# Performance work log

Hardware: AMD Instinct MI355X
Metric: run time of the kernel (lower is better)

The kernel has to match this reference:

```python
import jax, jax.numpy as jnp
import numpy as np

BS, DIM, EMB_DIM, SRC, TDEC, NEMB = 64, 512, 512, 400, 100, 50257


def intra_attention(h_t, h, W_attn):
    # h_t: [bs, dim]; h: [n, bs, dim]; W_attn: [dim, dim]
    n, bs, dim = h.shape
    # Faithful to torch .view([bs, dim, n]) on a contiguous [n, bs, dim]
    # tensor: raw row-major memory reinterpretation (NOT a transpose).
    hv = jnp.reshape(h, (bs, dim, n))  # [bs, dim, n]
    # E_t = (h_t @ W) [bs,1,dim] bmm hv [bs,dim,n] -> [bs, n]
    E = jnp.einsum('bd,bdn->bn', h_t @ W_attn, hv)
    # sum-normalized (non-softmax) score, eq. (4)
    A = E / jnp.sum(E, axis=1, keepdims=True)  # [bs, n]
    C = jnp.einsum('bdn,bn->bd', hv, A)        # [bs, dim]
    return A, C


def pointer_generator(ae_t, ce_t, hd_t, cd_t, W_emb, W_proj, W_u, b_u, b_out):
    # c_cat: [3*dim, bs]
    c_cat = jnp.concatenate((hd_t, ce_t, cd_t), axis=1).T
    # p_switch: [bs]
    p_switch = jax.nn.sigmoid(W_u @ c_cat + b_u).squeeze(0)
    # shared-embedding output projection, sect 2.4
    W_out = jnp.tanh(W_emb @ W_proj)           # [n_emb, 3*dim]
    logits = W_out @ c_cat + b_out             # [n_emb, bs]
    p_vocab = jax.nn.softmax(logits, axis=0)   # softmax over vocab
    p_gen = ((1.0 - p_switch) * p_vocab).T     # [bs, n_emb]
    p_copy = p_switch[:, None] * ae_t          # [bs, src]
    return p_gen, p_copy


def setup_inputs() -> dict:
    key = jax.random.key(0)
    ks = jax.random.split(key, 12)
    inp = {
        'h_t': jax.random.uniform(ks[0], (BS, DIM), dtype=jnp.float32),
        'h_enc': jax.random.uniform(ks[1], (SRC, BS, DIM), dtype=jnp.float32),
        'h_dec': jax.random.uniform(ks[2], (TDEC, BS, DIM), dtype=jnp.float32),
        'x': jax.random.randint(ks[3], (SRC, BS, 1), 0, NEMB, dtype=jnp.int64) if jax.config.jax_enable_x64 else jax.random.randint(ks[3], (SRC, BS, 1), 0, NEMB, dtype=jnp.int32),
        # positive attention weights keep the sum-normalized score well-conditioned
        'W_attn_enc': jax.random.uniform(ks[4], (DIM, DIM), dtype=jnp.float32, maxval=0.05),
        'W_attn_dec': jax.random.uniform(ks[5], (DIM, DIM), dtype=jnp.float32, maxval=0.05),
        'W_emb': jax.random.normal(ks[6], (NEMB, EMB_DIM), dtype=jnp.float32) * 0.02,
        'W_proj': jax.random.normal(ks[7], (EMB_DIM, 3 * DIM), dtype=jnp.float32) * 0.02,
        'W_u': jax.random.normal(ks[8], (1, 3 * DIM), dtype=jnp.float32) * 0.02,
        'b_u': jnp.zeros((1,), dtype=jnp.float32),
        'b_out': jnp.zeros((NEMB, 1), dtype=jnp.float32),
    }
    return inp


def reference(h_t, h_enc, h_dec, x, W_attn_enc, W_attn_dec, W_emb, W_proj, W_u, b_u, b_out):
    # one decode step of ReinforcedDecoder: enc attn + dec attn + pointer-gen
    ae_t, ce_t = intra_attention(h_t, h_enc, W_attn_enc)
    ad_t, cd_t = intra_attention(h_t, h_dec, W_attn_dec)
    p_gen, p_copy = pointer_generator(ae_t, ce_t, h_t, cd_t,
                                      W_emb, W_proj, W_u, b_u, b_out)
    return p_gen, p_copy
```

## Files before the change

kernel.cpp:

```cpp
#include <hip/hip_runtime.h>
#include <math.h>

typedef __attribute__((ext_vector_type(8))) short bf16x8;
typedef __attribute__((ext_vector_type(4))) float f32x4;
typedef __attribute__((ext_vector_type(4))) float f4v;

#define BS   64
#define DIM  512
#define SRC  400
#define TDEC 100
#define NEMB 50257
#define K3   1536

#define WS_Q     0
#define WS_EENC  65536
#define WS_EDEC  91136
#define WS_CENC  97536
#define WS_CDEC  130304
#define WS_ESUM  163072
#define WS_PSW   163200
#define WS_SMAX  163264
#define WS_SSUM  163520
#define WS_WPT   163776
#define WS_CCF   556992
#define WS_ZBEG  WS_CENC
#define WS_ZCNT  (WS_WPT - WS_CENC)

__device__ __forceinline__ ushort f2bf(float x) {
    union { float f; unsigned u; } v; v.f = x;
    unsigned r = (v.u + 0x7FFFu + ((v.u >> 16) & 1u)) >> 16;
    return (ushort)r;
}
__device__ __forceinline__ bf16x8 pack8v(f4v a, f4v b) {
    union { ushort us[8]; bf16x8 v; } p;
    p.us[0] = f2bf(a.x); p.us[1] = f2bf(a.y); p.us[2] = f2bf(a.z); p.us[3] = f2bf(a.w);
    p.us[4] = f2bf(b.x); p.us[5] = f2bf(b.y); p.us[6] = f2bf(b.z); p.us[7] = f2bf(b.w);
    return p.v;
}
__device__ __forceinline__ float pade_tanh(float x) {
    const float x2 = x * x;
    const float num = x * fmaf(x2, 1.0f / 15.0f, 1.0f);
    const float den = fmaf(x2, 0.4f, 1.0f);
    return num * __frcp_rn(den);
}
__device__ __forceinline__ void gl2lds16(const void* g, void* l) {
    __builtin_amdgcn_global_load_lds(
        (const __attribute__((address_space(1))) unsigned int*)g,
        (__attribute__((address_space(3))) unsigned int*)l, 16, 0, 0);
}

__global__ __launch_bounds__(256) void k_prep(const float* __restrict__ h_t,
                                              const float* __restrict__ Wenc,
                                              const float* __restrict__ Wdec,
                                              const float* __restrict__ Wp,
                                              float* __restrict__ ws) {
    __shared__ float sh[128 * 68];
    const int tid = threadIdx.x;
    if (blockIdx.x < 32) {
        const int which = blockIdx.x >> 4;
        const int c0 = (blockIdx.x & 15) * 32;
        const float* W = which ? Wdec : Wenc;
        float* q = ws + WS_Q + which * (BS * DIM);
        float* hS = sh;
        float* WSm = sh + 64 * 65;
        const int c = tid & 31, bg = tid >> 5;
        float acc[8] = {0.f, 0.f, 0.f, 0.f, 0.f, 0.f, 0.f, 0.f};
        for (int kc = 0; kc < 8; ++kc) {
            __syncthreads();
            #pragma unroll
            for (int r = 0; r < 16; ++r) {
                const int idx = r * 256 + tid;
                const int b = idx >> 6, k = idx & 63;
                hS[b * 65 + k] = h_t[b * DIM + kc * 64 + k];
            }
            #pragma unroll
            for (int r = 0; r < 8; ++r) {
                const int idx = r * 256 + tid;
                const int k = idx >> 5, cc = idx & 31;
                WSm[k * 33 + cc] = W[(size_t)(kc * 64 + k) * DIM + c0 + cc];
            }
            __syncthreads();
            #pragma unroll 8
            for (int k = 0; k < 64; ++k) {
                const float wv = WSm[k * 33 + c];
                #pragma unroll
                for (int bb = 0; bb < 8; ++bb)
                    acc[bb] = fmaf(hS[(bg * 8 + bb) * 65 + k], wv, acc[bb]);
            }
        }
        #pragma unroll
        for (int bb = 0; bb < 8; ++bb)
            q[(bg * 8 + bb) * DIM + c0 + c] = acc[bb];
    } else {
        const int bid = blockIdx.x - 32;
        const int t = bid >> 2, c = bid & 3;
        float (*T32)[68] = (float (*)[68])sh;
        #pragma unroll
        for (int p = 0; p < 8; ++p) {
            const int idx = p * 256 + tid;
            const int kk = idx >> 4, s = idx & 15;
            const float4 v = *(const float4*)(Wp + (size_t)(c * 128 + kk) * K3 + t * 64 + s * 4);
            T32[kk][s * 4 + 0] = v.x; T32[kk][s * 4 + 1] = v.y;
            T32[kk][s * 4 + 2] = v.z; T32[kk][s * 4 + 3] = v.w;
        }
        __syncthreads();
        char* dst = (char*)(ws + WS_WPT) + (size_t)bid * 16384;
        #pragma unroll
        for (int p = 0; p < 4; ++p) {
            const int fid = p * 256 + tid;
            const int lane = fid & 63;
            const int J = (fid >> 6) & 3;
            const int ks = fid >> 8;
            const int j = J * 16 + (lane & 15);
            const int k0 = ks * 32 + (lane >> 4) * 8;
            f4v a, b;
            a.x = T32[k0 + 0][j]; a.y = T32[k0 + 1][j];
            a.z = T32[k0 + 2][j]; a.w = T32[k0 + 3][j];
            b.x = T32[k0 + 4][j]; b.y = T32[k0 + 5][j];
            b.z = T32[k0 + 6][j]; b.w = T32[k0 + 7][j];
            *(bf16x8*)(dst + fid * 16) = pack8v(a, b);
        }
    }
}

#define IC 16
__global__ __launch_bounds__(256) void k_attn(const float* __restrict__ h_enc,
                                              const float* __restrict__ h_dec,
                                              float* __restrict__ ws) {
    const int b = blockIdx.x, which = blockIdx.y, z = blockIdx.z;
    const int tid = threadIdx.x;
    const int n   = which ? TDEC : SRC;
    const int per = which ? (TDEC / 4) : (SRC / 4);
    const int i_begin = z * per, i_end = i_begin + per;
    const float* h  = which ? h_dec : h_enc;
    const float* q  = ws + WS_Q + which * (BS * DIM) + b * DIM;
    float* wsE      = ws + (which ? WS_EDEC : WS_EENC) + b * n;
    float* Cws      = ws + (which ? WS_CDEC : WS_CENC) + b * DIM;
    const float* hb = h + (size_t)b * DIM * n;

    __shared__ float hS[DIM * (IC + 1)];
    __shared__ float qs[DIM];
    __shared__ float Ered[256];
    __shared__ float Es[IC];

    qs[tid] = q[tid];
    qs[tid + 256] = q[tid + 256];

    const int ii = tid & (IC - 1);
    const int dg = tid >> 4;
    float c0 = 0.f, c1 = 0.f, esum = 0.f;

    for (int i0 = i_begin; i0 < i_end; i0 += IC) {
        const int ic = min(IC, i_end - i0);
        __syncthreads();
        #pragma unroll 8
        for (int idx = tid; idx < DIM * IC; idx += 256) {
            const int d = idx >> 4, i = idx & (IC - 1);
            hS[d * (IC + 1) + i] = (i < ic) ? hb[(size_t)d * n + i0 + i] : 0.f;
        }
        __syncthreads();
        float p = 0.f;
        #pragma unroll 8
        for (int d = dg * 32; d < dg * 32 + 32; ++d) p += qs[d] * hS[d * (IC + 1) + ii];
        Ered[dg * IC + ii] = p;
        __syncthreads();
        if (tid < IC) {
            float e = 0.f;
            #pragma unroll
            for (int g = 0; g < 16; ++g) e += Ered[g * IC + tid];
            Es[tid] = e;
            esum += e;
            if (tid < ic) wsE[i0 + tid] = e;
        }
        __syncthreads();
        #pragma unroll
        for (int i = 0; i < IC; ++i) {
            const float e = Es[i];
            c0 += hS[tid * (IC + 1) + i] * e;
            c1 += hS[(tid + 256) * (IC + 1) + i] * e;
        }
    }
    atomicAdd(&Cws[tid], c0);
    atomicAdd(&Cws[tid + 256], c1);
    __syncthreads();
    if (tid < IC) Ered[tid] = esum;
    __syncthreads();
    if (tid == 0) {
        float s = 0.f;
        #pragma unroll
        for (int g = 0; g < IC; ++g) s += Ered[g];
        atomicAdd(&ws[WS_ESUM + which * 64 + b], s);
    }
}

__global__ void k_pswitch(const float* __restrict__ h_t,
                          const float* __restrict__ W_u,
                          const float* __restrict__ b_u,
                          float* __restrict__ out_copy,
                          float* __restrict__ ws) {
    const int b = blockIdx.x, tid = threadIdx.x;
    const float invE = 1.f / ws[WS_ESUM + b];
    const float invD = 1.f / ws[WS_ESUM + 64 + b];
    const float* Ce = ws + WS_CENC + b * DIM;
    const float* Cd = ws + WS_CDEC + b * DIM;
    ushort* ccF = (ushort*)(ws + WS_CCF);
    __shared__ float red[256];
    const int nb = b >> 4, bl = b & 15;
    float part = 0.f;
    #pragma unroll
    for (int r = 0; r < 6; ++r) {
        const int j = tid + r * 256;
        float v = (j < DIM) ? h_t[b * DIM + j]
                            : ((j < 2 * DIM) ? Ce[j - DIM] * invE : Cd[j - 2 * DIM] * invD);
        const int t = j >> 6, jj = j & 63;
        const int kc = jj >> 5, lsub = (jj >> 3) & 3, e = jj & 7;
        ccF[t * 4096 + kc * 2048 + nb * 512 + (lsub * 16 + bl) * 8 + e] = f2bf(v);
        part += W_u[j] * v;
    }
    red[tid] = part;
    __syncthreads();
    for (int s = 128; s > 0; s >>= 1) {
        if (tid < s) red[tid] += red[tid + s];
        __syncthreads();
    }
    const float ps = 1.f / (1.f + expf(-(red[0] + b_u[0])));
    if (tid == 0) ws[WS_PSW + b] = ps;
    const float* Ee = ws + WS_EENC + b * SRC;
    for (int i = tid; i < SRC; i += 256) out_copy[b * SRC + i] = ps * Ee[i] * invE;
}

#define VB 128
#define WAITV(N) asm volatile("s_waitcnt vmcnt(" #N ")" ::: "memory")
__global__ __launch_bounds__(256, 2) void k_bigmm(const float* __restrict__ We,
                                                  const float* __restrict__ ws,
                                                  const float* __restrict__ b_out,
                                                  float* __restrict__ out) {
    __shared__ __align__(16) char smem[57344];
    const char* wptb = (const char*)(ws + WS_WPT);
    const char* ccfb = (const char*)(ws + WS_CCF);

    const int tid  = threadIdx.x;
    const int w    = tid >> 6, lane = tid & 63;
    const int lrow = lane & 15, lgrp = lane >> 4;
    const int vw   = blockIdx.x * VB + w * 32;
    const int row0 = vw + lrow, row1 = vw + 16 + lrow;
    char* ccL   = smem + 32768;
    char* tbase = smem + 40960 + w * 4096;
    const int swz = (lrow & 7) << 4;

    #pragma unroll
    for (int p = 0; p < 2; ++p) {
        const char* src = wptb + (size_t)p * 16384 + tid * 16;
        char* dst = smem + p * 16384 + tid * 16;
        #pragma unroll
        for (int rnd = 0; rnd < 4; ++rnd) gl2lds16(src + rnd * 4096, dst + rnd * 4096);
    }

    bf16x8 A0[16], A1[16];
    if (row0 < NEMB) {
        const f4v* p = (const f4v*)(We + (size_t)row0 * DIM + lgrp * 8);
        #pragma unroll
        for (int f = 0; f < 16; ++f)
            A0[f] = pack8v(__builtin_nontemporal_load(p + f * 8),
                           __builtin_nontemporal_load(p + f * 8 + 1));
    } else {
        #pragma unroll
        for (int f = 0; f < 16; ++f) A0[f] = (bf16x8){0, 0, 0, 0, 0, 0, 0, 0};
    }
    if (row1 < NEMB) {
        const f4v* p = (const f4v*)(We + (size_t)row1 * DIM + lgrp * 8);
        #pragma unroll
        for (int f = 0; f < 16; ++f)
            A1[f] = pack8v(__builtin_nontemporal_load(p + f * 8),
                           __builtin_nontemporal_load(p + f * 8 + 1));
    } else {
        #pragma unroll
        for (int f = 0; f < 16; ++f) A1[f] = (bf16x8){0, 0, 0, 0, 0, 0, 0, 0};
    }

    f32x4 La0[4], La1[4], Ta0[4], Ta1[4];
    #pragma unroll
    for (int i = 0; i < 4; ++i) {
        La0[i] = (f32x4){0.f, 0.f, 0.f, 0.f}; La1[i] = (f32x4){0.f, 0.f, 0.f, 0.f};
        Ta0[i] = (f32x4){0.f, 0.f, 0.f, 0.f}; Ta1[i] = (f32x4){0.f, 0.f, 0.f, 0.f};
    }

    for (int it = 0; it < 8; ++it) {
        #pragma unroll
        for (int u = 0; u < 12; ++u) {
            const int i = it * 12 + u;
            if (u == 11)           { if (it == 7) { WAITV(0); } else { WAITV(4); } }
            else if ((u & 3) == 1) { WAITV(6); }
            else                   { WAITV(4); }
            __builtin_amdgcn_s_barrier();
            {
                const char* bp = smem + (u & 1) * 16384 + lane * 16;
                __builtin_amdgcn_s_setprio(1);
                #pragma unroll
                for (int ks = 0; ks < 4; ++ks) {
                    const bf16x8 b0 = *(const bf16x8*)(bp + ks * 4096);
                    const bf16x8 b1 = *(const bf16x8*)(bp + ks * 4096 + 1024);
                    const bf16x8 b2 = *(const bf16x8*)(bp + ks * 4096 + 2048);
                    const bf16x8 b3 = *(const bf16x8*)(bp + ks * 4096 + 3072);
                    Ta0[0] = __builtin_amdgcn_mfma_f32_16x16x32_bf16(A0[(u & 3) * 4 + ks], b0, Ta0[0], 0, 0, 0);
                    Ta1[0] = __builtin_amdgcn_mfma_f32_16x16x32_bf16(A1[(u & 3) * 4 + ks], b0, Ta1[0], 0, 0, 0);
                    Ta0[1] = __builtin_amdgcn_mfma_f32_16x16x32_bf16(A0[(u & 3) * 4 + ks], b1, Ta0[1], 0, 0, 0);
                    Ta1[1] = __builtin_amdgcn_mfma_f32_16x16x32_bf16(A1[(u & 3) * 4 + ks], b1, Ta1[1], 0, 0, 0);
                    Ta0[2] = __builtin_amdgcn_mfma_f32_16x16x32_bf16(A0[(u & 3) * 4 + ks], b2, Ta0[2], 0, 0, 0);
                    Ta1[2] = __builtin_amdgcn_mfma_f32_16x16x32_bf16(A1[(u & 3) * 4 + ks], b2, Ta1[2], 0, 0, 0);
                    Ta0[3] = __builtin_amdgcn_mfma_f32_16x16x32_bf16(A0[(u & 3) * 4 + ks], b3, Ta0[3], 0, 0, 0);
                    Ta1[3] = __builtin_amdgcn_mfma_f32_16x16x32_bf16(A1[(u & 3) * 4 + ks], b3, Ta1[3], 0, 0, 0);
                }
                __builtin_amdgcn_s_setprio(0);
            }
            if ((u & 3) == 3) {
                #pragma unroll
                for (int nj = 0; nj < 4; ++nj) {
                    const int j = nj * 16 + lrow;
                    #pragma unroll
                    for (int r = 0; r < 4; ++r) {
                        const int v = lgrp * 4 + r;
                        *(ushort*)(tbase + v * 128 + ((j * 2) ^ ((v & 7) << 4))) =
                            f2bf(pade_tanh(Ta0[nj][r]));
                        *(ushort*)(tbase + (16 + v) * 128 + ((j * 2) ^ ((v & 7) << 4))) =
                            f2bf(pade_tanh(Ta1[nj][r]));
                    }
                }
                __builtin_amdgcn_s_setprio(1);
                #pragma unroll
                for (int kc = 0; kc < 2; ++kc) {
                    const bf16x8 tf0 = *(const bf16x8*)(tbase + lrow * 128 +
                                                        ((kc * 64 + lgrp * 16) ^ swz));
                    const bf16x8 tf1 = *(const bf16x8*)(tbase + (16 + lrow) * 128 +
                                                        ((kc * 64 + lgrp * 16) ^ swz));
                    const char* cb = ccL + kc * 4096 + lane * 16;
                    const bf16x8 c0 = *(const bf16x8*)(cb);
                    const bf16x8 c1 = *(const bf16x8*)(cb + 1024);
                    const bf16x8 c2 = *(const bf16x8*)(cb + 2048);
                    const bf16x8 c3 = *(const bf16x8*)(cb + 3072);
                    La0[0] = __builtin_amdgcn_mfma_f32_16x16x32_bf16(tf0, c0, La0[0], 0, 0, 0);
                    La1[0] = __builtin_amdgcn_mfma_f32_16x16x32_bf16(tf1, c0, La1[0], 0, 0, 0);
                    La0[1] = __builtin_amdgcn_mfma_f32_16x16x32_bf16(tf0, c1, La0[1], 0, 0, 0);
                    La1[1] = __builtin_amdgcn_mfma_f32_16x16x32_bf16(tf1, c1, La1[1], 0, 0, 0);
                    La0[2] = __builtin_amdgcn_mfma_f32_16x16x32_bf16(tf0, c2, La0[2], 0, 0, 0);
                    La1[2] = __builtin_amdgcn_mfma_f32_16x16x32_bf16(tf1, c2, La1[2], 0, 0, 0);
                    La0[3] = __builtin_amdgcn_mfma_f32_16x16x32_bf16(tf0, c3, La0[3], 0, 0, 0);
                    La1[3] = __builtin_amdgcn_mfma_f32_16x16x32_bf16(tf1, c3, La1[3], 0, 0, 0);
                }
                __builtin_amdgcn_s_setprio(0);
                #pragma unroll
                for (int z = 0; z < 4; ++z) {
                    Ta0[z] = (f32x4){0.f, 0.f, 0.f, 0.f};
                    Ta1[z] = (f32x4){0.f, 0.f, 0.f, 0.f};
                }
            }
            __builtin_amdgcn_s_barrier();
            if ((u & 3) == 0) {
                const int t = it * 3 + (u >> 2);
                const char* csrc = ccfb + (size_t)t * 8192 + tid * 16;
                char* cdst = ccL + tid * 16;
                gl2lds16(csrc, cdst);
                gl2lds16(csrc + 4096, cdst + 4096);
            }
            if (i + 2 < 96) {
                const char* src = wptb + (size_t)(i + 2) * 16384 + tid * 16;
                char* dst = smem + (u & 1) * 16384 + tid * 16;
                #pragma unroll
                for (int rnd = 0; rnd < 4; ++rnd)
                    gl2lds16(src + rnd * 4096, dst + rnd * 4096);
            }
        }
    }

    #pragma unroll
    for (int nb = 0; nb < 4; ++nb) {
        const int b = nb * 16 + lrow;
        #pragma unroll
        for (int r = 0; r < 4; ++r) {
            const int v0 = vw + lgrp * 4 + r;
            const int v1 = v0 + 16;
            if (v0 < NEMB) out[(size_t)b * NEMB + v0] = La0[nb][r] + b_out[v0];
            if (v1 < NEMB) out[(size_t)b * NEMB + v1] = La1[nb][r] + b_out[v1];
        }
    }
}

#define VCC 12565
__global__ void k_colstat(const float* __restrict__ out, float* __restrict__ ws) {
    const int b = blockIdx.x, vc = blockIdx.y, tid = threadIdx.x;
    const float* L = out + (size_t)b * NEMB;
    const int v0 = vc * VCC, vend = min(v0 + VCC, NEMB);
    __shared__ float red[256];
    float m = -1e30f;
    for (int v = v0 + tid; v < vend; v += 256) m = fmaxf(m, L[v]);
    red[tid] = m;
    __syncthreads();
    for (int s = 128; s > 0; s >>= 1) {
        if (tid < s) red[tid] = fmaxf(red[tid], red[tid + s]);
        __syncthreads();
    }
    const float mb = red[0];
    __syncthreads();
    float sum = 0.f;
    for (int v = v0 + tid; v < vend; v += 256) sum += expf(L[v] - mb);
    red[tid] = sum;
    __syncthreads();
    for (int s = 128; s > 0; s >>= 1) {
        if (tid < s) red[tid] += red[tid + s];
        __syncthreads();
    }
    if (tid == 0) {
        ws[WS_SMAX + b * 4 + vc] = mb;
        ws[WS_SSUM + b * 4 + vc] = red[0];
    }
}

__global__ __launch_bounds__(256) void k_final(float* __restrict__ out,
                                               const float* __restrict__ ws) {
    const int b = blockIdx.x, seg = blockIdx.y, tid = threadIdx.x;
    float m = -1e30f;
    #pragma unroll
    for (int p = 0; p < 4; ++p) m = fmaxf(m, ws[WS_SMAX + b * 4 + p]);
    float s = 0.f;
    #pragma unroll
    for (int p = 0; p < 4; ++p)
        s += ws[WS_SSUM + b * 4 + p] * expf(ws[WS_SMAX + b * 4 + p] - m);
    const float scale = (1.f - ws[WS_PSW + b]) / s;
    float* L = out + (size_t)b * NEMB;
    const int v0 = seg * 3142, vend = min(v0 + 3142, NEMB);
    for (int v = v0 + tid; v < vend; v += 256) L[v] = expf(L[v] - m) * scale;
}

extern "C" void kernel_launch(void* const* d_in, const int* in_sizes, int n_in,
                              void* d_out, int out_size, void* d_ws, size_t ws_size,
                              hipStream_t stream) {
    const float* h_t        = (const float*)d_in[0];
    const float* h_enc      = (const float*)d_in[1];
    const float* h_dec      = (const float*)d_in[2];
    const float* W_attn_enc = (const float*)d_in[4];
    const float* W_attn_dec = (const float*)d_in[5];
    const float* W_emb      = (const float*)d_in[6];
    const float* W_proj     = (const float*)d_in[7];
    const float* W_u        = (const float*)d_in[8];
    const float* b_u        = (const float*)d_in[9];
    const float* b_out      = (const float*)d_in[10];

    float* out = (float*)d_out;
    float* ws  = (float*)d_ws;
    float* out_copy = out + (size_t)BS * NEMB;

    hipMemsetAsync(ws + WS_ZBEG, 0, (size_t)WS_ZCNT * sizeof(float), stream);
    k_prep   <<<128, 256, 0, stream>>>(h_t, W_attn_enc, W_attn_dec, W_proj, ws);
    k_attn   <<<dim3(64, 2, 4), 256, 0, stream>>>(h_enc, h_dec, ws);
    k_pswitch<<<64, 256, 0, stream>>>(h_t, W_u, b_u, out_copy, ws);
    k_bigmm  <<<(NEMB + VB - 1) / VB, 256, 0, stream>>>(W_emb, ws, b_out, out);
    k_colstat<<<dim3(64, 4), 256, 0, stream>>>(out, ws);
    k_final  <<<dim3(64, 16), 256, 0, stream>>>(out, ws);
}
```

Baseline: 306.4 us.

## Split big vocab GEMM over K halves with packed bf16 partial outputs

```diff
diff --git a/kernel.cpp b/kernel.cpp
--- a/kernel.cpp
+++ b/kernel.cpp
@@ -31,6 +31,9 @@
     unsigned r = (v.u + 0x7FFFu + ((v.u >> 16) & 1u)) >> 16;
     return (ushort)r;
 }
+__device__ __forceinline__ float bfdec(unsigned u16) {
+    return __uint_as_float(u16 << 16);
+}
 __device__ __forceinline__ bf16x8 pack8v(f4v a, f4v b) {
     union { ushort us[8]; bf16x8 v; } p;
     p.us[0] = f2bf(a.x); p.us[1] = f2bf(a.y); p.us[2] = f2bf(a.z); p.us[3] = f2bf(a.w);
@@ -56,6 +59,8 @@
                                               float* __restrict__ ws) {
     __shared__ float sh[128 * 68];
     const int tid = threadIdx.x;
+    for (int i = blockIdx.x * 256 + tid; i < WS_ZCNT; i += 128 * 256)
+        ws[WS_ZBEG + i] = 0.f;
     if (blockIdx.x < 32) {
         const int which = blockIdx.x >> 4;
         const int c0 = (blockIdx.x & 15) * 32;
@@ -124,14 +129,17 @@
 }
 
 #define IC 16
+#define NZ 8
 __global__ __launch_bounds__(256) void k_attn(const float* __restrict__ h_enc,
                                               const float* __restrict__ h_dec,
                                               float* __restrict__ ws) {
     const int b = blockIdx.x, which = blockIdx.y, z = blockIdx.z;
     const int tid = threadIdx.x;
     const int n   = which ? TDEC : SRC;
-    const int per = which ? (TDEC / 4) : (SRC / 4);
-    const int i_begin = z * per, i_end = i_begin + per;
+    const int per = (n + NZ - 1) / NZ;
+    const int i_begin = z * per;
+    const int i_end = min(n, i_begin + per);
+    if (i_begin >= n) return;
     const float* h  = which ? h_dec : h_enc;
     const float* q  = ws + WS_Q + which * (BS * DIM) + b * DIM;
     float* wsE      = ws + (which ? WS_EDEC : WS_EENC) + b * n;
@@ -230,22 +238,23 @@
 }
 
 #define VB 128
+#define NTILE ((NEMB + VB - 1) / VB)
 #define WAITV(N) asm volatile("s_waitcnt vmcnt(" #N ")" ::: "memory")
-__global__ __launch_bounds__(256, 2) void k_bigmm(const float* __restrict__ We,
+__global__ __launch_bounds__(256, 3) void k_bigmm(const float* __restrict__ We,
                                                   const float* __restrict__ ws,
-                                                  const float* __restrict__ b_out,
                                                   float* __restrict__ out) {
-    __shared__ __align__(16) char smem[57344];
-    const char* wptb = (const char*)(ws + WS_WPT);
-    const char* ccfb = (const char*)(ws + WS_CCF);
+    __shared__ __align__(16) char smem[49152];
+    const int tile = blockIdx.x >> 1, half = blockIdx.x & 1;
+    const char* wptb = (const char*)(ws + WS_WPT) + (size_t)half * 48 * 16384;
+    const char* ccfb = (const char*)(ws + WS_CCF) + (size_t)half * 12 * 8192;
 
     const int tid  = threadIdx.x;
     const int w    = tid >> 6, lane = tid & 63;
     const int lrow = lane & 15, lgrp = lane >> 4;
-    const int vw   = blockIdx.x * VB + w * 32;
+    const int vw   = tile * VB + w * 32;
     const int row0 = vw + lrow, row1 = vw + 16 + lrow;
     char* ccL   = smem + 32768;
-    char* tbase = smem + 40960 + w * 4096;
+    char* tbase = smem + 40960 + w * 2048;
     const int swz = (lrow & 7) << 4;
 
     #pragma unroll
@@ -285,11 +294,11 @@
         Ta0[i] = (f32x4){0.f, 0.f, 0.f, 0.f}; Ta1[i] = (f32x4){0.f, 0.f, 0.f, 0.f};
     }
 
-    for (int it = 0; it < 8; ++it) {
+    for (int it = 0; it < 4; ++it) {
         #pragma unroll
         for (int u = 0; u < 12; ++u) {
             const int i = it * 12 + u;
-            if (u == 11)           { if (it == 7) { WAITV(0); } else { WAITV(4); } }
+            if (u == 11)           { if (it == 3) { WAITV(0); } else { WAITV(4); } }
             else if ((u & 3) == 1) { WAITV(6); }
             else                   { WAITV(4); }
             __builtin_amdgcn_s_barrier();
@@ -314,6 +323,15 @@
                 __builtin_amdgcn_s_setprio(0);
             }
             if ((u & 3) == 3) {
+                const bf16x8 c00 = *(const bf16x8*)(ccL + lane * 16);
+                const bf16x8 c01 = *(const bf16x8*)(ccL + lane * 16 + 1024);
+                const bf16x8 c02 = *(const bf16x8*)(ccL + lane * 16 + 2048);
+                const bf16x8 c03 = *(const bf16x8*)(ccL + lane * 16 + 3072);
+                const bf16x8 c10 = *(const bf16x8*)(ccL + 4096 + lane * 16);
+                const bf16x8 c11 = *(const bf16x8*)(ccL + 4096 + lane * 16 + 1024);
+                const bf16x8 c12 = *(const bf16x8*)(ccL + 4096 + lane * 16 + 2048);
+                const bf16x8 c13 = *(const bf16x8*)(ccL + 4096 + lane * 16 + 3072);
+                __builtin_amdgcn_s_setprio(1);
                 #pragma unroll
                 for (int nj = 0; nj < 4; ++nj) {
                     const int j = nj * 16 + lrow;
@@ -322,30 +340,41 @@
                         const int v = lgrp * 4 + r;
                         *(ushort*)(tbase + v * 128 + ((j * 2) ^ ((v & 7) << 4))) =
                             f2bf(pade_tanh(Ta0[nj][r]));
-                        *(ushort*)(tbase + (16 + v) * 128 + ((j * 2) ^ ((v & 7) << 4))) =
+                    }
+                }
+                {
+                    const bf16x8 tfa = *(const bf16x8*)(tbase + lrow * 128 + ((lgrp * 16) ^ swz));
+                    const bf16x8 tfb = *(const bf16x8*)(tbase + lrow * 128 + ((64 + lgrp * 16) ^ swz));
+                    La0[0] = __builtin_amdgcn_mfma_f32_16x16x32_bf16(tfa, c00, La0[0], 0, 0, 0);
+                    La0[1] = __builtin_amdgcn_mfma_f32_16x16x32_bf16(tfa, c01, La0[1], 0, 0, 0);
+                    La0[2] = __builtin_amdgcn_mfma_f32_16x16x32_bf16(tfa, c02, La0[2], 0, 0, 0);
+                    La0[3] = __builtin_amdgcn_mfma_f32_16x16x32_bf16(tfa, c03, La0[3], 0, 0, 0);
+                    La0[0] = __builtin_amdgcn_mfma_f32_16x16x32_bf16(tfb, c10, La0[0], 0, 0, 0);
+                    La0[1] = __builtin_amdgcn_mfma_f32_16x16x32_bf16(tfb, c11, La0[1], 0, 0, 0);
+                    La0[2] = __builtin_amdgcn_mfma_f32_16x16x32_bf16(tfb, c12, La0[2], 0, 0, 0);
+                    La0[3] = __builtin_amdgcn_mfma_f32_16x16x32_bf16(tfb, c13, La0[3], 0, 0, 0);
+                }
+                #pragma unroll
+                for (int nj = 0; nj < 4; ++nj) {
+                    const int j = nj * 16 + lrow;
+                    #pragma unroll
+                    for (int r = 0; r < 4; ++r) {
+                        const int v = lgrp * 4 + r;
+                        *(ushort*)(tbase + v * 128 + ((j * 2) ^ ((v & 7) << 4))) =
                             f2bf(pade_tanh(Ta1[nj][r]));
                     }
                 }
-                __builtin_amdgcn_s_setprio(1);
-                #pragma unroll
-                for (int kc = 0; kc < 2; ++kc) {
-                    const bf16x8 tf0 = *(const bf16x8*)(tbase + lrow * 128 +
-                                                        ((kc * 64 + lgrp * 16) ^ swz));
-                    const bf16x8 tf1 = *(const bf16x8*)(tbase + (16 + lrow) * 128 +
-                                                        ((kc * 64 + lgrp * 16) ^ swz));
-                    const char* cb = ccL + kc * 4096 + lane * 16;
-                    const bf16x8 c0 = *(const bf16x8*)(cb);
-                    const bf16x8 c1 = *(const bf16x8*)(cb + 1024);
-                    const bf16x8 c2 = *(const bf16x8*)(cb + 2048);
-                    const bf16x8 c3 = *(const bf16x8*)(cb + 3072);
-                    La0[0] = __builtin_amdgcn_mfma_f32_16x16x32_bf16(tf0, c0, La0[0], 0, 0, 0);
-                    La1[0] = __builtin_amdgcn_mfma_f32_16x16x32_bf16(tf1, c0, La1[0], 0, 0, 0);
-                    La0[1] = __builtin_amdgcn_mfma_f32_16x16x32_bf16(tf0, c1, La0[1], 0, 0, 0);
-                    La1[1] = __builtin_amdgcn_mfma_f32_16x16x32_bf16(tf1, c1, La1[1], 0, 0, 0);
-                    La0[2] = __builtin_amdgcn_mfma_f32_16x16x32_bf16(tf0, c2, La0[2], 0, 0, 0);
-                    La1[2] = __builtin_amdgcn_mfma_f32_16x16x32_bf16(tf1, c2, La1[2], 0, 0, 0);
-                    La0[3] = __builtin_amdgcn_mfma_f32_16x16x32_bf16(tf0, c3, La0[3], 0, 0, 0);
-                    La1[3] = __builtin_amdgcn_mfma_f32_16x16x32_bf16(tf1, c3, La1[3], 0, 0, 0);
+                {
+                    const bf16x8 tfa = *(const bf16x8*)(tbase + lrow * 128 + ((lgrp * 16) ^ swz));
+                    const bf16x8 tfb = *(const bf16x8*)(tbase + lrow * 128 + ((64 + lgrp * 16) ^ swz));
+                    La1[0] = __builtin_amdgcn_mfma_f32_16x16x32_bf16(tfa, c00, La1[0], 0, 0, 0);
+                    La1[1] = __builtin_amdgcn_mfma_f32_16x16x32_bf16(tfa, c01, La1[1], 0, 0, 0);
+                    La1[2] = __builtin_amdgcn_mfma_f32_16x16x32_bf16(tfa, c02, La1[2], 0, 0, 0);
+                    La1[3] = __builtin_amdgcn_mfma_f32_16x16x32_bf16(tfa, c03, La1[3], 0, 0, 0);
+                    La1[0] = __builtin_amdgcn_mfma_f32_16x16x32_bf16(tfb, c10, La1[0], 0, 0, 0);
+                    La1[1] = __builtin_amdgcn_mfma_f32_16x16x32_bf16(tfb, c11, La1[1], 0, 0, 0);
+                    La1[2] = __builtin_amdgcn_mfma_f32_16x16x32_bf16(tfb, c12, La1[2], 0, 0, 0);
+                    La1[3] = __builtin_amdgcn_mfma_f32_16x16x32_bf16(tfb, c13, La1[3], 0, 0, 0);
                 }
                 __builtin_amdgcn_s_setprio(0);
                 #pragma unroll
@@ -362,7 +391,7 @@
                 gl2lds16(csrc, cdst);
                 gl2lds16(csrc + 4096, cdst + 4096);
             }
-            if (i + 2 < 96) {
+            if (i + 2 < 48) {
                 const char* src = wptb + (size_t)(i + 2) * 16384 + tid * 16;
                 char* dst = smem + (u & 1) * 16384 + tid * 16;
                 #pragma unroll
@@ -372,6 +401,7 @@
         }
     }
 
+    ushort* o16 = (ushort*)out;
     #pragma unroll
     for (int nb = 0; nb < 4; ++nb) {
         const int b = nb * 16 + lrow;
@@ -379,20 +409,25 @@
         for (int r = 0; r < 4; ++r) {
             const int v0 = vw + lgrp * 4 + r;
             const int v1 = v0 + 16;
-            if (v0 < NEMB) out[(size_t)b * NEMB + v0] = La0[nb][r] + b_out[v0];
-            if (v1 < NEMB) out[(size_t)b * NEMB + v1] = La1[nb][r] + b_out[v1];
+            if (v0 < NEMB) o16[((size_t)b * NEMB + v0) * 2 + half] = f2bf(La0[nb][r]);
+            if (v1 < NEMB) o16[((size_t)b * NEMB + v1) * 2 + half] = f2bf(La1[nb][r]);
         }
     }
 }
 
 #define VCC 12565
-__global__ void k_colstat(const float* __restrict__ out, float* __restrict__ ws) {
+__global__ void k_colstat(const float* __restrict__ out,
+                          const float* __restrict__ b_out,
+                          float* __restrict__ ws) {
     const int b = blockIdx.x, vc = blockIdx.y, tid = threadIdx.x;
-    const float* L = out + (size_t)b * NEMB;
+    const unsigned* L = (const unsigned*)(out + (size_t)b * NEMB);
     const int v0 = vc * VCC, vend = min(v0 + VCC, NEMB);
     __shared__ float red[256];
     float m = -1e30f;
-    for (int v = v0 + tid; v < vend; v += 256) m = fmaxf(m, L[v]);
+    for (int v = v0 + tid; v < vend; v += 256) {
+        const unsigned wrd = L[v];
+        m = fmaxf(m, bfdec(wrd & 0xFFFFu) + bfdec(wrd >> 16) + b_out[v]);
+    }
     red[tid] = m;
     __syncthreads();
     for (int s = 128; s > 0; s >>= 1) {
@@ -402,7 +437,10 @@
     const float mb = red[0];
     __syncthreads();
     float sum = 0.f;
-    for (int v = v0 + tid; v < vend; v += 256) sum += expf(L[v] - mb);
+    for (int v = v0 + tid; v < vend; v += 256) {
+        const unsigned wrd = L[v];
+        sum += expf(bfdec(wrd & 0xFFFFu) + bfdec(wrd >> 16) + b_out[v] - mb);
+    }
     red[tid] = sum;
     __syncthreads();
     for (int s = 128; s > 0; s >>= 1) {
@@ -416,6 +454,7 @@
 }
 
 __global__ __launch_bounds__(256) void k_final(float* __restrict__ out,
+                                               const float* __restrict__ b_out,
                                                const float* __restrict__ ws) {
     const int b = blockIdx.x, seg = blockIdx.y, tid = threadIdx.x;
     float m = -1e30f;
@@ -428,7 +467,11 @@
     const float scale = (1.f - ws[WS_PSW + b]) / s;
     float* L = out + (size_t)b * NEMB;
     const int v0 = seg * 3142, vend = min(v0 + 3142, NEMB);
-    for (int v = v0 + tid; v < vend; v += 256) L[v] = expf(L[v] - m) * scale;
+    for (int v = v0 + tid; v < vend; v += 256) {
+        const unsigned wrd = __float_as_uint(L[v]);
+        const float lg = bfdec(wrd & 0xFFFFu) + bfdec(wrd >> 16) + b_out[v];
+        L[v] = expf(lg - m) * scale;
+    }
 }
 
 extern "C" void kernel_launch(void* const* d_in, const int* in_sizes, int n_in,
@@ -449,11 +492,10 @@
     float* ws  = (float*)d_ws;
     float* out_copy = out + (size_t)BS * NEMB;
 
-    hipMemsetAsync(ws + WS_ZBEG, 0, (size_t)WS_ZCNT * sizeof(float), stream);
     k_prep   <<<128, 256, 0, stream>>>(h_t, W_attn_enc, W_attn_dec, W_proj, ws);
-    k_attn   <<<dim3(64, 2, 4), 256, 0, stream>>>(h_enc, h_dec, ws);
+    k_attn   <<<dim3(64, 2, NZ), 256, 0, stream>>>(h_enc, h_dec, ws);
     k_pswitch<<<64, 256, 0, stream>>>(h_t, W_u, b_u, out_copy, ws);
-    k_bigmm  <<<(NEMB + VB - 1) / VB, 256, 0, stream>>>(W_emb, ws, b_out, out);
-    k_colstat<<<dim3(64, 4), 256, 0, stream>>>(out, ws);
-    k_final  <<<dim3(64, 16), 256, 0, stream>>>(out, ws);
-}
+    k_bigmm  <<<2 * NTILE, 256, 0, stream>>>(W_emb, ws, out);
+    k_colstat<<<dim3(64, 4), 256, 0, stream>>>(out, b_out, ws);
+    k_final  <<<dim3(64, 16), 256, 0, stream>>>(out, b_out, ws);
+}
```

After: 561.8 us. 83.4% more time.
